# Performance work log

Measured on AMD Instinct MI355X. Metric: run time of the kernel, lower is better.

The kernel has to match this reference:

```python
import jax, jax.numpy as jnp
import numpy as np

H = 64  # LSTM hidden size

def _lstm_layer(x, Wih, Whh, bih, bhh):
    # x: [B,T,I]; PyTorch gate order (i, f, g, o); zero initial state
    B, T, _ = x.shape
    pre = jnp.einsum('bti,gi->btg', x, Wih) + bih + bhh  # [B,T,4H]
    def step(carry, p):
        h, c = carry
        g = p + h @ Whh.T
        i, f, gg, o = jnp.split(g, 4, axis=-1)
        c = jax.nn.sigmoid(f) * c + jax.nn.sigmoid(i) * jnp.tanh(gg)
        h = jax.nn.sigmoid(o) * jnp.tanh(c)
        return (h, c), h
    h0 = jnp.zeros((B, H), x.dtype)
    c0 = jnp.zeros((B, H), x.dtype)
    _, hs = jax.lax.scan(step, (h0, c0), jnp.swapaxes(pre, 0, 1))
    return jnp.swapaxes(hs, 0, 1)  # [B,T,H]

def _lstm_params(key, in_dim):
    s = 1.0 / np.sqrt(H)
    k1, k2, k3, k4 = jax.random.split(key, 4)
    return (jax.random.uniform(k1, (4 * H, in_dim), jnp.float32, -s, s),
            jax.random.uniform(k2, (4 * H, H), jnp.float32, -s, s),
            jax.random.uniform(k3, (4 * H,), jnp.float32, -s, s),
            jax.random.uniform(k4, (4 * H,), jnp.float32, -s, s))

def setup_inputs() -> dict:
    key = jax.random.key(0)
    ks = jax.random.split(key, 9)
    B, T = 1024, 1024
    x = jax.random.normal(ks[0], (B, T, 3), jnp.float32)
    e1 = _lstm_params(ks[1], 3)
    e2 = _lstm_params(ks[2], H)
    d1 = _lstm_params(ks[3], 5)
    d2 = _lstm_params(ks[4], H)
    s = 1.0 / np.sqrt(H)
    enc_fc_W = jax.random.uniform(ks[5], (5, H), jnp.float32, -s, s)
    enc_fc_b = jax.random.uniform(ks[6], (5,), jnp.float32, -s, s)
    dec_fc_W = jax.random.uniform(ks[7], (3, H), jnp.float32, -s, s)
    dec_fc_b = jax.random.uniform(ks[8], (3,), jnp.float32, -s, s)
    return {
        'x': x,
        'e1_Wih': e1[0], 'e1_Whh': e1[1], 'e1_bih': e1[2], 'e1_bhh': e1[3],
        'e2_Wih': e2[0], 'e2_Whh': e2[1], 'e2_bih': e2[2], 'e2_bhh': e2[3],
        'enc_fc_W': enc_fc_W, 'enc_fc_b': enc_fc_b,
        'd1_Wih': d1[0], 'd1_Whh': d1[1], 'd1_bih': d1[2], 'd1_bhh': d1[3],
        'd2_Wih': d2[0], 'd2_Whh': d2[1], 'd2_bih': d2[2], 'd2_bhh': d2[3],
        'dec_fc_W': dec_fc_W, 'dec_fc_b': dec_fc_b,
    }

def reference(x,
              e1_Wih, e1_Whh, e1_bih, e1_bhh,
              e2_Wih, e2_Whh, e2_bih, e2_bhh,
              enc_fc_W, enc_fc_b,
              d1_Wih, d1_Whh, d1_bih, d1_bhh,
              d2_Wih, d2_Whh, d2_bih, d2_bhh,
              dec_fc_W, dec_fc_b):
    h = _lstm_layer(x, e1_Wih, e1_Whh, e1_bih, e1_bhh)
    h = _lstm_layer(h, e2_Wih, e2_Whh, e2_bih, e2_bhh)
    u = h[:, -1, :] @ enc_fc_W.T + enc_fc_b        # [B,5]
    u = u[:, None, :]                               # [B,1,5]
    d = _lstm_layer(u, d1_Wih, d1_Whh, d1_bih, d1_bhh)
    d = _lstm_layer(d, d2_Wih, d2_Whh, d2_bih, d2_bhh)
    tau = d[:, -1, :] @ dec_fc_W.T + dec_fc_b       # [B,3]
    return (u, tau)
```

## Files before the change

### kernel.cpp

```cpp
#include <hip/hip_runtime.h>
#include <stdint.h>

typedef _Float16 f16x8 __attribute__((ext_vector_type(8)));
typedef float f32x4 __attribute__((ext_vector_type(4)));

__device__ __forceinline__ float sigf(float x) {
    return __builtin_amdgcn_rcpf(1.0f + __expf(-x));
}
__device__ __forceinline__ float tanhf_fast(float x) {
    return 1.0f - 2.0f * __builtin_amdgcn_rcpf(1.0f + __expf(2.0f * x));
}

__global__ __launch_bounds__(512, 1)
void lstm_mfma(const float* __restrict__ x,
               const float* __restrict__ W1i, const float* __restrict__ W1h,
               const float* __restrict__ b1i, const float* __restrict__ b1h,
               const float* __restrict__ W2i, const float* __restrict__ W2h,
               const float* __restrict__ b2i, const float* __restrict__ b2h,
               const float* __restrict__ eW,  const float* __restrict__ eb,
               const float* __restrict__ D1i, const float* __restrict__ D1bi,
               const float* __restrict__ D1bh,
               const float* __restrict__ D2i, const float* __restrict__ D2bi,
               const float* __restrict__ D2bh,
               const float* __restrict__ dW,  const float* __restrict__ db,
               float* __restrict__ out)
{
    __shared__ __align__(16) _Float16 h1b[2][16][104];
    __shared__ __align__(16) _Float16 h2b[16][72];
    __shared__ __align__(16) float preX[8][4][4][16];
    __shared__ float uL[4][8];
    __shared__ float tl1[4][64];
    __shared__ float tl2[4][64];

    const int tid = threadIdx.x, blk = blockIdx.x;
    const int wid = tid >> 6, lane = tid & 63;
    const int rl = lane & 15, hi = lane >> 4;
    const bool isL1 = (wid < 4);
    const int w = isL1 ? wid : wid - 4;

    {
        uint32_t* z1 = (uint32_t*)&h1b[0][0][0];
        for (int i = tid; i < 1664; i += 512) z1[i] = 0u;
        uint32_t* z2 = (uint32_t*)&h2b[0][0];
        for (int i = tid; i < 576; i += 512) z2[i] = 0u;
    }

    f16x8 afr[4][4];
    #pragma unroll
    for (int g = 0; g < 4; ++g) {
        const int grow = g * 64 + w * 16 + rl;
        if (isL1) {
            #pragma unroll
            for (int s = 0; s < 2; ++s) {
                f16x8 v;
                #pragma unroll
                for (int i = 0; i < 8; ++i)
                    v[i] = (_Float16)W1h[grow * 64 + s * 32 + hi * 8 + i];
                afr[g][s] = v;
            }
            {
                f16x8 v;
                #pragma unroll
                for (int i = 0; i < 8; ++i) {
                    int kk = hi * 8 + i;
                    v[i] = (kk < 3) ? (_Float16)W1i[grow * 3 + kk] : (_Float16)0.0f;
                }
                afr[g][2] = v;
            }
            {
                f16x8 v;
                #pragma unroll
                for (int i = 0; i < 8; ++i) v[i] = (_Float16)0.0f;
                afr[g][3] = v;
            }
        } else {
            #pragma unroll
            for (int s = 0; s < 2; ++s) {
                f16x8 v;
                #pragma unroll
                for (int i = 0; i < 8; ++i)
                    v[i] = (_Float16)W2i[grow * 64 + s * 32 + hi * 8 + i];
                afr[g][s] = v;
            }
            #pragma unroll
            for (int s = 0; s < 2; ++s) {
                f16x8 v;
                #pragma unroll
                for (int i = 0; i < 8; ++i)
                    v[i] = (_Float16)W2h[grow * 64 + s * 32 + hi * 8 + i];
                afr[g][2 + s] = v;
            }
        }
    }

    f32x4 bias[4];
    #pragma unroll
    for (int g = 0; g < 4; ++g) {
        #pragma unroll
        for (int r = 0; r < 4; ++r) {
            int grow = g * 64 + w * 16 + hi * 4 + r;
            bias[g][r] = isL1 ? (b1i[grow] + b1h[grow]) : (b2i[grow] + b2h[grow]);
        }
    }

    float cst = 0.0f;

    __syncthreads();
    if (wid == 0 && lane < 4) {
        const float* xp = x + (size_t)(blk * 4 + lane) * 3072;
        h1b[0][lane][64] = (_Float16)xp[0];
        h1b[0][lane][65] = (_Float16)xp[1];
        h1b[0][lane][66] = (_Float16)xp[2];
    }
    __syncthreads();

    #pragma unroll 1
    for (int t = 0; t <= 1024; ++t) {
        const int p = t & 1;
        const bool doL1 = isL1 && (t < 1024);
        const bool doL2 = (!isL1) && (t >= 1);

        if (doL1) {
            f32x4 a0 = bias[0], a1 = bias[1], a2 = bias[2], a3 = bias[3];
            #pragma unroll
            for (int s = 0; s < 3; ++s) {
                f16x8 bf = *(const f16x8*)&h1b[p][rl][s * 32 + hi * 8];
                a0 = __builtin_amdgcn_mfma_f32_16x16x32_f16(afr[0][s], bf, a0, 0, 0, 0);
                a1 = __builtin_amdgcn_mfma_f32_16x16x32_f16(afr[1][s], bf, a1, 0, 0, 0);
                a2 = __builtin_amdgcn_mfma_f32_16x16x32_f16(afr[2][s], bf, a2, 0, 0, 0);
                a3 = __builtin_amdgcn_mfma_f32_16x16x32_f16(afr[3][s], bf, a3, 0, 0, 0);
            }
            if (rl < 4) {
                *(f32x4*)&preX[wid][0][rl][hi * 4] = a0;
                *(f32x4*)&preX[wid][1][rl][hi * 4] = a1;
                *(f32x4*)&preX[wid][2][rl][hi * 4] = a2;
                *(f32x4*)&preX[wid][3][rl][hi * 4] = a3;
            }
        } else if (doL2) {
            f32x4 a0 = bias[0], a1 = bias[1], a2 = bias[2], a3 = bias[3];
            #pragma unroll
            for (int s = 0; s < 2; ++s) {
                f16x8 bf = *(const f16x8*)&h1b[p][rl][s * 32 + hi * 8];
                a0 = __builtin_amdgcn_mfma_f32_16x16x32_f16(afr[0][s], bf, a0, 0, 0, 0);
                a1 = __builtin_amdgcn_mfma_f32_16x16x32_f16(afr[1][s], bf, a1, 0, 0, 0);
                a2 = __builtin_amdgcn_mfma_f32_16x16x32_f16(afr[2][s], bf, a2, 0, 0, 0);
                a3 = __builtin_amdgcn_mfma_f32_16x16x32_f16(afr[3][s], bf, a3, 0, 0, 0);
            }
            #pragma unroll
            for (int s = 0; s < 2; ++s) {
                f16x8 bf = *(const f16x8*)&h2b[rl][s * 32 + hi * 8];
                a0 = __builtin_amdgcn_mfma_f32_16x16x32_f16(afr[0][2 + s], bf, a0, 0, 0, 0);
                a1 = __builtin_amdgcn_mfma_f32_16x16x32_f16(afr[1][2 + s], bf, a1, 0, 0, 0);
                a2 = __builtin_amdgcn_mfma_f32_16x16x32_f16(afr[2][2 + s], bf, a2, 0, 0, 0);
                a3 = __builtin_amdgcn_mfma_f32_16x16x32_f16(afr[3][2 + s], bf, a3, 0, 0, 0);
            }
            if (rl < 4) {
                *(f32x4*)&preX[wid][0][rl][hi * 4] = a0;
                *(f32x4*)&preX[wid][1][rl][hi * 4] = a1;
                *(f32x4*)&preX[wid][2][rl][hi * 4] = a2;
                *(f32x4*)&preX[wid][3][rl][hi * 4] = a3;
            }
        }
        __syncthreads();

        if (doL1 || doL2) {
            float pi  = preX[wid][0][hi][rl];
            float pf  = preX[wid][1][hi][rl];
            float pgg = preX[wid][2][hi][rl];
            float po  = preX[wid][3][hi][rl];
            cst = sigf(pf) * cst + sigf(pi) * tanhf_fast(pgg);
            float hn = sigf(po) * tanhf_fast(cst);
            if (doL1) h1b[p ^ 1][hi][w * 16 + rl] = (_Float16)hn;
            else      h2b[hi][w * 16 + rl] = (_Float16)hn;
        }
        if (wid == 0 && lane < 4 && (t + 1) < 1024) {
            const float* xp = x + (size_t)(blk * 4 + lane) * 3072 + (size_t)(t + 1) * 3;
            h1b[p ^ 1][lane][64] = (_Float16)xp[0];
            h1b[p ^ 1][lane][65] = (_Float16)xp[1];
            h1b[p ^ 1][lane][66] = (_Float16)xp[2];
        }
        __syncthreads();
    }

    const int S = blk * 4 + wid;
    if (tid < 256 && lane < 5) {
        float acc = eb[lane];
        for (int k = 0; k < 64; ++k) acc += eW[lane * 64 + k] * (float)h2b[wid][k];
        uL[wid][lane] = acc;
        out[S * 5 + lane] = acc;
    }
    __syncthreads();

    if (tid < 256) {
        float u0 = uL[wid][0], u1 = uL[wid][1], u2 = uL[wid][2], u3 = uL[wid][3], u4 = uL[wid][4];
        int ri = lane, rg = 128 + lane, ro = 192 + lane;
        float pi = D1bi[ri] + D1bh[ri];
        float pg = D1bi[rg] + D1bh[rg];
        float po = D1bi[ro] + D1bh[ro];
        pi += D1i[ri*5+0]*u0 + D1i[ri*5+1]*u1 + D1i[ri*5+2]*u2 + D1i[ri*5+3]*u3 + D1i[ri*5+4]*u4;
        pg += D1i[rg*5+0]*u0 + D1i[rg*5+1]*u1 + D1i[rg*5+2]*u2 + D1i[rg*5+3]*u3 + D1i[rg*5+4]*u4;
        po += D1i[ro*5+0]*u0 + D1i[ro*5+1]*u1 + D1i[ro*5+2]*u2 + D1i[ro*5+3]*u3 + D1i[ro*5+4]*u4;
        float cd = sigf(pi) * tanhf_fast(pg);
        float hd = sigf(po) * tanhf_fast(cd);
        tl1[wid][lane] = hd;
    }
    __syncthreads();

    if (tid < 256) {
        int ri = lane, rg = 128 + lane, ro = 192 + lane;
        float pi = D2bi[ri] + D2bh[ri];
        float pg = D2bi[rg] + D2bh[rg];
        float po = D2bi[ro] + D2bh[ro];
        for (int k = 0; k < 64; ++k) {
            float hk = tl1[wid][k];
            pi += D2i[ri * 64 + k] * hk;
            pg += D2i[rg * 64 + k] * hk;
            po += D2i[ro * 64 + k] * hk;
        }
        float cd = sigf(pi) * tanhf_fast(pg);
        float hd = sigf(po) * tanhf_fast(cd);
        tl2[wid][lane] = hd;
    }
    __syncthreads();

    if (tid < 256 && lane < 3) {
        float acc = db[lane];
        for (int k = 0; k < 64; ++k) acc += dW[lane * 64 + k] * tl2[wid][k];
        out[5120 + S * 3 + lane] = acc;
    }
}

extern "C" void kernel_launch(void* const* d_in, const int* in_sizes, int n_in,
                              void* d_out, int out_size, void* d_ws, size_t ws_size,
                              hipStream_t stream) {
    (void)in_sizes; (void)n_in; (void)out_size; (void)d_ws; (void)ws_size;
    const float* x    = (const float*)d_in[0];
    const float* W1i  = (const float*)d_in[1];
    const float* W1h  = (const float*)d_in[2];
    const float* b1i  = (const float*)d_in[3];
    const float* b1h  = (const float*)d_in[4];
    const float* W2i  = (const float*)d_in[5];
    const float* W2h  = (const float*)d_in[6];
    const float* b2i  = (const float*)d_in[7];
    const float* b2h  = (const float*)d_in[8];
    const float* eW   = (const float*)d_in[9];
    const float* eb   = (const float*)d_in[10];
    const float* D1i  = (const float*)d_in[11];
    const float* D1bi = (const float*)d_in[13];
    const float* D1bh = (const float*)d_in[14];
    const float* D2i  = (const float*)d_in[15];
    const float* D2bi = (const float*)d_in[17];
    const float* D2bh = (const float*)d_in[18];
    const float* dW   = (const float*)d_in[19];
    const float* db   = (const float*)d_in[20];

    hipLaunchKernelGGL(lstm_mfma, dim3(256), dim3(512), 0, stream,
                       x, W1i, W1h, b1i, b1h, W2i, W2h, b2i, b2h, eW, eb,
                       D1i, D1bi, D1bh, D2i, D2bi, D2bh, dW, db,
                       (float*)d_out);
}
```

Measured before the change: 910.1 us.

## Pack 16 sequences per block and compute gate activations directly from MFMA registers

```diff
diff --git a/kernel.cpp b/kernel.cpp
--- a/kernel.cpp
+++ b/kernel.cpp
@@ -12,25 +12,24 @@
 }
 
 __global__ __launch_bounds__(512, 1)
-void lstm_mfma(const float* __restrict__ x,
-               const float* __restrict__ W1i, const float* __restrict__ W1h,
-               const float* __restrict__ b1i, const float* __restrict__ b1h,
-               const float* __restrict__ W2i, const float* __restrict__ W2h,
-               const float* __restrict__ b2i, const float* __restrict__ b2h,
-               const float* __restrict__ eW,  const float* __restrict__ eb,
-               const float* __restrict__ D1i, const float* __restrict__ D1bi,
-               const float* __restrict__ D1bh,
-               const float* __restrict__ D2i, const float* __restrict__ D2bi,
-               const float* __restrict__ D2bh,
-               const float* __restrict__ dW,  const float* __restrict__ db,
-               float* __restrict__ out)
+void lstm_mfma16(const float* __restrict__ x,
+                 const float* __restrict__ W1i, const float* __restrict__ W1h,
+                 const float* __restrict__ b1i, const float* __restrict__ b1h,
+                 const float* __restrict__ W2i, const float* __restrict__ W2h,
+                 const float* __restrict__ b2i, const float* __restrict__ b2h,
+                 const float* __restrict__ eW,  const float* __restrict__ eb,
+                 const float* __restrict__ D1i, const float* __restrict__ D1bi,
+                 const float* __restrict__ D1bh,
+                 const float* __restrict__ D2i, const float* __restrict__ D2bi,
+                 const float* __restrict__ D2bh,
+                 const float* __restrict__ dW,  const float* __restrict__ db,
+                 float* __restrict__ out)
 {
     __shared__ __align__(16) _Float16 h1b[2][16][104];
-    __shared__ __align__(16) _Float16 h2b[16][72];
-    __shared__ __align__(16) float preX[8][4][4][16];
-    __shared__ float uL[4][8];
-    __shared__ float tl1[4][64];
-    __shared__ float tl2[4][64];
+    __shared__ __align__(16) _Float16 h2b[2][16][72];
+    __shared__ float uW[8][8];
+    __shared__ float tlA[8][64];
+    __shared__ float tlB[8][64];
 
     const int tid = threadIdx.x, blk = blockIdx.x;
     const int wid = tid >> 6, lane = tid & 63;
@@ -41,8 +40,8 @@
     {
         uint32_t* z1 = (uint32_t*)&h1b[0][0][0];
         for (int i = tid; i < 1664; i += 512) z1[i] = 0u;
-        uint32_t* z2 = (uint32_t*)&h2b[0][0];
-        for (int i = tid; i < 576; i += 512) z2[i] = 0u;
+        uint32_t* z2 = (uint32_t*)&h2b[0][0][0];
+        for (int i = tid; i < 1152; i += 512) z2[i] = 0u;
     }
 
     f16x8 afr[4][4];
@@ -103,11 +102,11 @@
         }
     }
 
-    float cst = 0.0f;
+    float cst[4] = {0.0f, 0.0f, 0.0f, 0.0f};
 
     __syncthreads();
-    if (wid == 0 && lane < 4) {
-        const float* xp = x + (size_t)(blk * 4 + lane) * 3072;
+    if (wid == 0 && lane < 16) {
+        const float* xp = x + (size_t)(blk * 16 + lane) * 3072;
         h1b[0][lane][64] = (_Float16)xp[0];
         h1b[0][lane][65] = (_Float16)xp[1];
         h1b[0][lane][66] = (_Float16)xp[2];
@@ -117,10 +116,15 @@
     #pragma unroll 1
     for (int t = 0; t <= 1024; ++t) {
         const int p = t & 1;
-        const bool doL1 = isL1 && (t < 1024);
-        const bool doL2 = (!isL1) && (t >= 1);
-
-        if (doL1) {
+
+        float xf0 = 0.f, xf1 = 0.f, xf2 = 0.f;
+        const bool doX = (wid == 0) && (lane < 16) && (t + 1 < 1024);
+        if (doX) {
+            const float* xp = x + (size_t)(blk * 16 + lane) * 3072 + (size_t)(t + 1) * 3;
+            xf0 = xp[0]; xf1 = xp[1]; xf2 = xp[2];
+        }
+
+        if (isL1 && t < 1024) {
             f32x4 a0 = bias[0], a1 = bias[1], a2 = bias[2], a3 = bias[3];
             #pragma unroll
             for (int s = 0; s < 3; ++s) {
@@ -130,13 +134,19 @@
                 a2 = __builtin_amdgcn_mfma_f32_16x16x32_f16(afr[2][s], bf, a2, 0, 0, 0);
                 a3 = __builtin_amdgcn_mfma_f32_16x16x32_f16(afr[3][s], bf, a3, 0, 0, 0);
             }
-            if (rl < 4) {
-                *(f32x4*)&preX[wid][0][rl][hi * 4] = a0;
-                *(f32x4*)&preX[wid][1][rl][hi * 4] = a1;
-                *(f32x4*)&preX[wid][2][rl][hi * 4] = a2;
-                *(f32x4*)&preX[wid][3][rl][hi * 4] = a3;
-            }
-        } else if (doL2) {
+            uint16_t hu[4];
+            #pragma unroll
+            for (int r = 0; r < 4; ++r) {
+                float pi = a0[r], pf = a1[r], pgg = a2[r], po = a3[r];
+                cst[r] = sigf(pf) * cst[r] + sigf(pi) * tanhf_fast(pgg);
+                float hn = sigf(po) * tanhf_fast(cst[r]);
+                hu[r] = __builtin_bit_cast(uint16_t, (_Float16)hn);
+            }
+            uint2 pk;
+            pk.x = (uint32_t)hu[0] | ((uint32_t)hu[1] << 16);
+            pk.y = (uint32_t)hu[2] | ((uint32_t)hu[3] << 16);
+            *(uint2*)&h1b[p ^ 1][rl][w * 16 + hi * 4] = pk;
+        } else if (!isL1 && t >= 1) {
             f32x4 a0 = bias[0], a1 = bias[1], a2 = bias[2], a3 = bias[3];
             #pragma unroll
             for (int s = 0; s < 2; ++s) {
@@ -148,85 +158,87 @@
             }
             #pragma unroll
             for (int s = 0; s < 2; ++s) {
-                f16x8 bf = *(const f16x8*)&h2b[rl][s * 32 + hi * 8];
+                f16x8 bf = *(const f16x8*)&h2b[p][rl][s * 32 + hi * 8];
                 a0 = __builtin_amdgcn_mfma_f32_16x16x32_f16(afr[0][2 + s], bf, a0, 0, 0, 0);
                 a1 = __builtin_amdgcn_mfma_f32_16x16x32_f16(afr[1][2 + s], bf, a1, 0, 0, 0);
                 a2 = __builtin_amdgcn_mfma_f32_16x16x32_f16(afr[2][2 + s], bf, a2, 0, 0, 0);
                 a3 = __builtin_amdgcn_mfma_f32_16x16x32_f16(afr[3][2 + s], bf, a3, 0, 0, 0);
             }
-            if (rl < 4) {
-                *(f32x4*)&preX[wid][0][rl][hi * 4] = a0;
-                *(f32x4*)&preX[wid][1][rl][hi * 4] = a1;
-                *(f32x4*)&preX[wid][2][rl][hi * 4] = a2;
-                *(f32x4*)&preX[wid][3][rl][hi * 4] = a3;
-            }
-        }
-        __syncthreads();
-
-        if (doL1 || doL2) {
-            float pi  = preX[wid][0][hi][rl];
-            float pf  = preX[wid][1][hi][rl];
-            float pgg = preX[wid][2][hi][rl];
-            float po  = preX[wid][3][hi][rl];
-            cst = sigf(pf) * cst + sigf(pi) * tanhf_fast(pgg);
-            float hn = sigf(po) * tanhf_fast(cst);
-            if (doL1) h1b[p ^ 1][hi][w * 16 + rl] = (_Float16)hn;
-            else      h2b[hi][w * 16 + rl] = (_Float16)hn;
-        }
-        if (wid == 0 && lane < 4 && (t + 1) < 1024) {
-            const float* xp = x + (size_t)(blk * 4 + lane) * 3072 + (size_t)(t + 1) * 3;
-            h1b[p ^ 1][lane][64] = (_Float16)xp[0];
-            h1b[p ^ 1][lane][65] = (_Float16)xp[1];
-            h1b[p ^ 1][lane][66] = (_Float16)xp[2];
-        }
-        __syncthreads();
-    }
-
-    const int S = blk * 4 + wid;
-    if (tid < 256 && lane < 5) {
-        float acc = eb[lane];
-        for (int k = 0; k < 64; ++k) acc += eW[lane * 64 + k] * (float)h2b[wid][k];
-        uL[wid][lane] = acc;
-        out[S * 5 + lane] = acc;
-    }
-    __syncthreads();
-
-    if (tid < 256) {
-        float u0 = uL[wid][0], u1 = uL[wid][1], u2 = uL[wid][2], u3 = uL[wid][3], u4 = uL[wid][4];
-        int ri = lane, rg = 128 + lane, ro = 192 + lane;
-        float pi = D1bi[ri] + D1bh[ri];
-        float pg = D1bi[rg] + D1bh[rg];
-        float po = D1bi[ro] + D1bh[ro];
-        pi += D1i[ri*5+0]*u0 + D1i[ri*5+1]*u1 + D1i[ri*5+2]*u2 + D1i[ri*5+3]*u3 + D1i[ri*5+4]*u4;
-        pg += D1i[rg*5+0]*u0 + D1i[rg*5+1]*u1 + D1i[rg*5+2]*u2 + D1i[rg*5+3]*u3 + D1i[rg*5+4]*u4;
-        po += D1i[ro*5+0]*u0 + D1i[ro*5+1]*u1 + D1i[ro*5+2]*u2 + D1i[ro*5+3]*u3 + D1i[ro*5+4]*u4;
-        float cd = sigf(pi) * tanhf_fast(pg);
-        float hd = sigf(po) * tanhf_fast(cd);
-        tl1[wid][lane] = hd;
-    }
-    __syncthreads();
-
-    if (tid < 256) {
-        int ri = lane, rg = 128 + lane, ro = 192 + lane;
-        float pi = D2bi[ri] + D2bh[ri];
-        float pg = D2bi[rg] + D2bh[rg];
-        float po = D2bi[ro] + D2bh[ro];
-        for (int k = 0; k < 64; ++k) {
-            float hk = tl1[wid][k];
-            pi += D2i[ri * 64 + k] * hk;
-            pg += D2i[rg * 64 + k] * hk;
-            po += D2i[ro * 64 + k] * hk;
-        }
-        float cd = sigf(pi) * tanhf_fast(pg);
-        float hd = sigf(po) * tanhf_fast(cd);
-        tl2[wid][lane] = hd;
-    }
-    __syncthreads();
-
-    if (tid < 256 && lane < 3) {
-        float acc = db[lane];
-        for (int k = 0; k < 64; ++k) acc += dW[lane * 64 + k] * tl2[wid][k];
-        out[5120 + S * 3 + lane] = acc;
+            uint16_t hu[4];
+            #pragma unroll
+            for (int r = 0; r < 4; ++r) {
+                float pi = a0[r], pf = a1[r], pgg = a2[r], po = a3[r];
+                cst[r] = sigf(pf) * cst[r] + sigf(pi) * tanhf_fast(pgg);
+                float hn = sigf(po) * tanhf_fast(cst[r]);
+                hu[r] = __builtin_bit_cast(uint16_t, (_Float16)hn);
+            }
+            uint2 pk;
+            pk.x = (uint32_t)hu[0] | ((uint32_t)hu[1] << 16);
+            pk.y = (uint32_t)hu[2] | ((uint32_t)hu[3] << 16);
+            *(uint2*)&h2b[p ^ 1][rl][w * 16 + hi * 4] = pk;
+        }
+
+        if (doX) {
+            h1b[p ^ 1][lane][64] = (_Float16)xf0;
+            h1b[p ^ 1][lane][65] = (_Float16)xf1;
+            h1b[p ^ 1][lane][66] = (_Float16)xf2;
+        }
+        __syncthreads();
+    }
+
+    #pragma unroll 1
+    for (int ss = 0; ss < 2; ++ss) {
+        const int s = wid * 2 + ss;
+        const int S = blk * 16 + s;
+
+        if (lane < 5) {
+            float acc = eb[lane];
+            for (int k = 0; k < 64; ++k)
+                acc += eW[lane * 64 + k] * (float)h2b[1][s][k];
+            uW[wid][lane] = acc;
+            out[S * 5 + lane] = acc;
+        }
+        __syncthreads();
+
+        {
+            float u0 = uW[wid][0], u1 = uW[wid][1], u2 = uW[wid][2],
+                  u3 = uW[wid][3], u4 = uW[wid][4];
+            int ri = lane, rg = 128 + lane, ro = 192 + lane;
+            float pi = D1bi[ri] + D1bh[ri];
+            float pg = D1bi[rg] + D1bh[rg];
+            float po = D1bi[ro] + D1bh[ro];
+            pi += D1i[ri*5+0]*u0 + D1i[ri*5+1]*u1 + D1i[ri*5+2]*u2 + D1i[ri*5+3]*u3 + D1i[ri*5+4]*u4;
+            pg += D1i[rg*5+0]*u0 + D1i[rg*5+1]*u1 + D1i[rg*5+2]*u2 + D1i[rg*5+3]*u3 + D1i[rg*5+4]*u4;
+            po += D1i[ro*5+0]*u0 + D1i[ro*5+1]*u1 + D1i[ro*5+2]*u2 + D1i[ro*5+3]*u3 + D1i[ro*5+4]*u4;
+            float cd = sigf(pi) * tanhf_fast(pg);
+            float hd = sigf(po) * tanhf_fast(cd);
+            tlA[wid][lane] = hd;
+        }
+        __syncthreads();
+
+        {
+            int ri = lane, rg = 128 + lane, ro = 192 + lane;
+            float pi = D2bi[ri] + D2bh[ri];
+            float pg = D2bi[rg] + D2bh[rg];
+            float po = D2bi[ro] + D2bh[ro];
+            for (int k = 0; k < 64; ++k) {
+                float hk = tlA[wid][k];
+                pi += D2i[ri * 64 + k] * hk;
+                pg += D2i[rg * 64 + k] * hk;
+                po += D2i[ro * 64 + k] * hk;
+            }
+            float cd = sigf(pi) * tanhf_fast(pg);
+            float hd = sigf(po) * tanhf_fast(cd);
+            tlB[wid][lane] = hd;
+        }
+        __syncthreads();
+
+        if (lane < 3) {
+            float acc = db[lane];
+            for (int k = 0; k < 64; ++k) acc += dW[lane * 64 + k] * tlB[wid][k];
+            out[5120 + S * 3 + lane] = acc;
+        }
+        __syncthreads();
     }
 }
 
@@ -254,7 +266,7 @@
     const float* dW   = (const float*)d_in[19];
     const float* db   = (const float*)d_in[20];
 
-    hipLaunchKernelGGL(lstm_mfma, dim3(256), dim3(512), 0, stream,
+    hipLaunchKernelGGL(lstm_mfma16, dim3(64), dim3(512), 0, stream,
                        x, W1i, W1h, b1i, b1h, W2i, W2h, b2i, b2h, eW, eb,
                        D1i, D1bi, D1bh, D2i, D2bi, D2bh, dW, db,
                        (float*)d_out);
```

New measurement: 1.007 ms. +10.7%, slower.
